# Optimization experiments

Hardware: AMD Instinct MI355X
Metric: run time of the kernel (lower is better)

## Reference

```python
import jax, jax.numpy as jnp
import numpy as np

C = 1.0      # base manifold curvature (Lorentz c)
C_E = 1.0    # expert manifold curvature (all experts init to c=1.0)
K = 1        # n_activated_experts (top-k)
SCALE = 2.0  # LResNet scale for shared-expert combine
EPS = 1e-8


def _lorentz_swiglu(x, W1, W3, W2, c_mid, c_out, prescale):
    """LorentzExpert / LorentzFeedForward: SwiGLU on space coords with Lorentz time lift.
    x: [T, D] (full Lorentz vector). W1,W3: [I-1, D]; W2: [D-1, I]. Returns [T, D]."""
    if prescale:
        x = x * np.float32(np.sqrt(C_E / C))  # x * sqrt(c_expert / c)
    s1 = jax.nn.silu(x @ W1.T)                 # [T, I-1] w1(x, return_space=True)
    s3 = x @ W3.T                              # [T, I-1] w3(x, return_space=True)
    sp = s1 * s3                               # gated space part
    t = jnp.sqrt(jnp.clip((sp * sp).sum(-1, keepdims=True) + c_mid, EPS))
    h = jnp.concatenate([t, sp], axis=-1)      # [T, I] point on expert manifold
    o = h @ W2.T                               # [T, D-1] w2 space output
    ot = jnp.sqrt(jnp.clip((o * o).sum(-1, keepdims=True) + c_out, EPS))
    return jnp.concatenate([ot, o], axis=-1)   # [T, D] on base manifold


def setup_inputs() -> dict:
    key = jax.random.key(0)
    ks = jax.random.split(key, 9)
    T, D, E, I = 2048, 1024, 8, 1024
    x = jax.random.normal(ks[0], (T, D), jnp.float32)
    gate_w = jax.random.normal(ks[1], (E, D - 1), jnp.float32) / np.sqrt(D - 1)
    gate_b = jax.random.normal(ks[2], (E,), jnp.float32) * 0.01
    W1 = jax.random.normal(ks[3], (E, I - 1, D), jnp.float32) / np.sqrt(D)
    W3 = jax.random.normal(ks[4], (E, I - 1, D), jnp.float32) / np.sqrt(D)
    W2 = jax.random.normal(ks[5], (E, D - 1, I), jnp.float32) / np.sqrt(I)
    Ws1 = jax.random.normal(ks[6], (I - 1, D), jnp.float32) / np.sqrt(D)
    Ws3 = jax.random.normal(ks[7], (I - 1, D), jnp.float32) / np.sqrt(D)
    Ws2 = jax.random.normal(ks[8], (D - 1, I), jnp.float32) / np.sqrt(I)
    return {"x": x, "gate_w": gate_w, "gate_b": gate_b, "W1": W1, "W3": W3,
            "W2": W2, "Ws1": Ws1, "Ws3": Ws3, "Ws2": Ws2}


def reference(x, gate_w, gate_b, W1, W3, W2, Ws1, Ws3, Ws2):
    T, D = x.shape
    E = gate_w.shape[0]
    # ---- Gate (softmax scoring, n_groups == 1, route_scale == 1.0) ----
    logits = x[:, 1:] @ gate_w.T                                    # [T, E]
    scores = jax.nn.softmax(logits.astype(jnp.float32), axis=-1)
    biased = scores + gate_b                                        # bias only affects routing
    _, idx = jax.lax.top_k(biased, K)                               # [T, K]
    weights = jnp.take_along_axis(scores, idx, axis=-1).astype(x.dtype)  # [T, K]
    # dense per-token expert gate weights [T, E]
    oh = jax.nn.one_hot(idx, E, dtype=x.dtype)                      # [T, K, E]
    gw = (oh * weights[..., None]).sum(axis=1)                      # [T, E]
    # ---- y init: project(zeros) -> [sqrt(c), 0, ..., 0] ----
    y0 = jnp.concatenate([jnp.full((T, 1), np.sqrt(C), x.dtype),
                          jnp.zeros((T, D - 1), x.dtype)], axis=-1)
    # ---- routed experts (dense reference: every expert on every token, masked combine) ----
    e_out = jax.vmap(lambda w1, w3, w2: _lorentz_swiglu(x, w1, w3, w2, C_E, C, True))(W1, W3, W2)  # [E, T, D]
    y = y0 + jnp.einsum('te,etd->td', gw, e_out)
    # ---- shared expert (LorentzFeedForward, stays on base manifold) ----
    z = _lorentz_swiglu(x, Ws1, Ws3, Ws2, C, C, False)
    # ---- LResNet weighted sum: normalize (z + scale*y) back to manifold ----
    comb = z + SCALE * y
    li = (comb[:, 1:] ** 2).sum(-1, keepdims=True) - comb[:, :1] ** 2  # Lorentz inner <comb,comb>
    out = np.float32(np.sqrt(C)) * comb / jnp.sqrt(jnp.clip(jnp.abs(li), EPS))
    return out
```

## Files before the change

kernel.cpp:

```cpp
#include <hip/hip_runtime.h>

typedef __bf16 bf16;
typedef __attribute__((ext_vector_type(8))) __bf16 bf16x8;
typedef __attribute__((ext_vector_type(4))) float floatx4;

#define TOK 2048
#define DD  1024
#define NE  8
#define LDA 40
#define MAXSLOT 72

__device__ __forceinline__ uint4 pack_bf8(float4 a, float4 b) {
  union { bf16 h[8]; uint4 u; } p;
  p.h[0] = (bf16)a.x; p.h[1] = (bf16)a.y; p.h[2] = (bf16)a.z; p.h[3] = (bf16)a.w;
  p.h[4] = (bf16)b.x; p.h[5] = (bf16)b.y; p.h[6] = (bf16)b.z; p.h[7] = (bf16)b.w;
  return p.u;
}

__global__ __launch_bounds__(256) void gate_cvt_kernel(
    const float* __restrict__ x, const float* __restrict__ gate_w,
    const float* __restrict__ gate_b, bf16* __restrict__ x_bf,
    int* __restrict__ eidx, float* __restrict__ ewgt)
{
  const int t = blockIdx.x, tid = threadIdx.x;
  const float4 v = ((const float4*)(x + (size_t)t * DD))[tid];
  union { bf16 h[4]; uint2 u; } pk;
  pk.h[0] = (bf16)v.x; pk.h[1] = (bf16)v.y; pk.h[2] = (bf16)v.z; pk.h[3] = (bf16)v.w;
  ((uint2*)(x_bf + (size_t)t * DD))[tid] = pk.u;

  float acc[NE];
#pragma unroll
  for (int e = 0; e < NE; ++e) acc[e] = 0.f;
  const float vv[4] = {v.x, v.y, v.z, v.w};
#pragma unroll
  for (int i = 0; i < 4; ++i) {
    const int d = tid * 4 + i;
    if (d >= 1) {
#pragma unroll
      for (int e = 0; e < NE; ++e) acc[e] += vv[i] * gate_w[e * (DD - 1) + d - 1];
    }
  }
#pragma unroll
  for (int off = 32; off > 0; off >>= 1) {
#pragma unroll
    for (int e = 0; e < NE; ++e) acc[e] += __shfl_down(acc[e], off);
  }
  __shared__ float red[4][NE];
  const int wid = tid >> 6, lane = tid & 63;
  if (lane == 0) {
#pragma unroll
    for (int e = 0; e < NE; ++e) red[wid][e] = acc[e];
  }
  __syncthreads();
  if (tid == 0) {
    float lg[NE];
#pragma unroll
    for (int e = 0; e < NE; ++e) lg[e] = red[0][e] + red[1][e] + red[2][e] + red[3][e];
    float m = lg[0];
    for (int e = 1; e < NE; ++e) m = fmaxf(m, lg[e]);
    float ex[NE], s = 0.f;
    for (int e = 0; e < NE; ++e) { ex[e] = expf(lg[e] - m); s += ex[e]; }
    const float inv = 1.f / s;
    int best = 0; float bb = ex[0] * inv + gate_b[0];
    for (int e = 1; e < NE; ++e) {
      const float b = ex[e] * inv + gate_b[e];
      if (b > bb) { bb = b; best = e; }
    }
    eidx[t] = best;
    ewgt[t] = ex[best] * inv;
  }
}

__global__ __launch_bounds__(256) void route_kernel(
    const int* __restrict__ eidx, int* __restrict__ perm,
    int* __restrict__ pos_of, int4* __restrict__ wl, int* __restrict__ wl_n)
{
  __shared__ int cnt[NE], off[NE], bas[NE + 1];
  const int tid = threadIdx.x;
  if (tid < NE) cnt[tid] = 0;
  __syncthreads();
  for (int t = tid; t < TOK; t += 256) atomicAdd(&cnt[eidx[t]], 1);
  __syncthreads();
  if (tid == 0) {
    int run = 0;
    for (int e = 0; e < NE; ++e) { bas[e] = run; off[e] = run; run += cnt[e]; }
    bas[NE] = run;
    int n = 0;
    for (int e = 0; e < NE; ++e)
      for (int r0 = 0; r0 < cnt[e]; r0 += 64) {
        int rows = cnt[e] - r0; if (rows > 64) rows = 64;
        wl[n++] = make_int4(bas[e] + r0, rows, e, 0);
      }
    for (int r0 = 0; r0 < TOK; r0 += 64) wl[n++] = make_int4(r0, 64, NE, 0);
    *wl_n = n;
  }
  __syncthreads();
  for (int t = tid; t < TOK; t += 256) {
    const int e = eidx[t];
    const int p = atomicAdd(&off[e], 1);
    perm[p] = t;
    pos_of[t] = p;
  }
}

__global__ __launch_bounds__(256) void mlp1_kernel(
    const bf16* __restrict__ x_bf,
    const float* __restrict__ W1, const float* __restrict__ W3,
    const float* __restrict__ Ws1, const float* __restrict__ Ws3,
    const int* __restrict__ perm, const int4* __restrict__ wl,
    const int* __restrict__ wl_n,
    bf16* __restrict__ h_r, bf16* __restrict__ h_s,
    float* __restrict__ ss_r, float* __restrict__ ss_z)
{
  const int bid = blockIdx.x;
  const int slot = bid >> 4, nt = bid & 15;
  if (slot >= *wl_n) return;
  const int4 wle = wl[slot];
  const int mbase = wle.x, rows = wle.y, eid = wle.z;
  const int tid = threadIdx.x;
  const bool routed = (eid < NE);
  const float* w1p = routed ? W1 + (size_t)eid * 1023 * 1024 : Ws1;
  const float* w3p = routed ? W3 + (size_t)eid * 1023 * 1024 : Ws3;
  bf16* hbuf  = routed ? h_r : h_s;
  float* ssbuf = routed ? ss_r : ss_z;
  const int n0 = nt * 64;

  __shared__ __align__(16) bf16 As[64 * LDA];
  __shared__ __align__(16) bf16 B1s[64 * LDA];
  __shared__ __align__(16) bf16 B3s[64 * LDA];
  __shared__ int toks[64];

  if (tid < 64) {
    int r = tid < rows ? tid : rows - 1;
    toks[tid] = routed ? perm[mbase + r] : (mbase + r);
  }
  __syncthreads();

  const int arow = tid >> 2, acol = (tid & 3) * 8;
  const bf16* aptr = x_bf + (size_t)toks[arow] * DD + acol;
  bf16* const alds = As + arow * LDA + acol;

  const int brow = tid >> 2, bcol = (tid & 3) * 8;
  int bn = n0 + brow; if (bn > 1022) bn = 1022;
  const float* b1ptr = w1p + (size_t)bn * 1024 + bcol;
  const float* b3ptr = w3p + (size_t)bn * 1024 + bcol;
  bf16* const b1lds = B1s + brow * LDA + bcol;
  bf16* const b3lds = B3s + brow * LDA + bcol;

  const int wid = tid >> 6, lane = tid & 63;
  const int wc = wid * 16;
  const int lrow = lane & 15, quad = lane >> 4;

  const floatx4 fz = {0.f, 0.f, 0.f, 0.f};
  floatx4 acc1[4], acc3[4];
#pragma unroll
  for (int mi = 0; mi < 4; ++mi) { acc1[mi] = fz; acc3[mi] = fz; }

  uint4  a0  = *(const uint4*)(aptr);
  float4 f10 = *(const float4*)(b1ptr);
  float4 f11 = *(const float4*)(b1ptr + 4);
  float4 f30 = *(const float4*)(b3ptr);
  float4 f31 = *(const float4*)(b3ptr + 4);

  for (int k0 = 0; k0 < 1024; k0 += 32) {
    __syncthreads();
    *(uint4*)alds  = a0;
    *(uint4*)b1lds = pack_bf8(f10, f11);
    *(uint4*)b3lds = pack_bf8(f30, f31);
    __syncthreads();
    const int kn = (k0 + 32 < 1024) ? (k0 + 32) : 0;
    a0  = *(const uint4*)(aptr + kn);
    f10 = *(const float4*)(b1ptr + kn);
    f11 = *(const float4*)(b1ptr + kn + 4);
    f30 = *(const float4*)(b3ptr + kn);
    f31 = *(const float4*)(b3ptr + kn + 4);

    bf16x8 af[4], b1f, b3f;
#pragma unroll
    for (int mi = 0; mi < 4; ++mi)
      af[mi] = *(const bf16x8*)(As + (mi * 16 + lrow) * LDA + quad * 8);
    b1f = *(const bf16x8*)(B1s + (wc + lrow) * LDA + quad * 8);
    b3f = *(const bf16x8*)(B3s + (wc + lrow) * LDA + quad * 8);
#pragma unroll
    for (int mi = 0; mi < 4; ++mi) {
      acc1[mi] = __builtin_amdgcn_mfma_f32_16x16x32_bf16(af[mi], b1f, acc1[mi], 0, 0, 0);
      acc3[mi] = __builtin_amdgcn_mfma_f32_16x16x32_bf16(af[mi], b3f, acc3[mi], 0, 0, 0);
    }
  }

  const int n = n0 + wc + lrow;
#pragma unroll
  for (int mi = 0; mi < 4; ++mi) {
#pragma unroll
    for (int r = 0; r < 4; ++r) {
      const int row = mi * 16 + quad * 4 + r;
      const bool ok = (row < rows) && (n < 1023);
      const float s1 = acc1[mi][r];
      const float s3 = acc3[mi][r];
      const float sp = (s1 / (1.f + __expf(-s1))) * s3;
      float ssum = ok ? sp * sp : 0.f;
      if (ok) hbuf[(size_t)(mbase + row) * 1024 + 1 + n] = (bf16)sp;
      ssum += __shfl_xor(ssum, 1);
      ssum += __shfl_xor(ssum, 2);
      ssum += __shfl_xor(ssum, 4);
      ssum += __shfl_xor(ssum, 8);
      if (lrow == 0 && row < rows) atomicAdd(ssbuf + mbase + row, ssum);
    }
  }
}

__global__ __launch_bounds__(256) void finalize_t_kernel(
    const float* __restrict__ ss_r, const float* __restrict__ ss_z,
    bf16* __restrict__ h_r, bf16* __restrict__ h_s)
{
  const int i = blockIdx.x * 256 + threadIdx.x;
  if (i < TOK) {
    h_r[(size_t)i * 1024] = (bf16)sqrtf(ss_r[i] + 1.0f);
    h_s[(size_t)i * 1024] = (bf16)sqrtf(ss_z[i] + 1.0f);
  }
}

__global__ __launch_bounds__(256) void mlp2_kernel(
    const bf16* __restrict__ h_r, const bf16* __restrict__ h_s,
    const float* __restrict__ W2, const float* __restrict__ Ws2,
    const int4* __restrict__ wl, const int* __restrict__ wl_n,
    float* __restrict__ o_r, float* __restrict__ o_s,
    float* __restrict__ ss_or, float* __restrict__ ss_oz)
{
  const int bid = blockIdx.x;
  const int slot = bid >> 4, nt = bid & 15;
  if (slot >= *wl_n) return;
  const int4 wle = wl[slot];
  const int mbase = wle.x, rows = wle.y, eid = wle.z;
  const int tid = threadIdx.x;
  const bool routed = (eid < NE);
  const float* wp = routed ? W2 + (size_t)eid * 1023 * 1024 : Ws2;
  const bf16* abuf = routed ? h_r : h_s;
  float* obuf  = routed ? o_r : o_s;
  float* ssbuf = routed ? ss_or : ss_oz;
  const int n0 = nt * 64;

  __shared__ __align__(16) bf16 As[64 * LDA];
  __shared__ __align__(16) bf16 Bs[64 * LDA];

  const int arow = tid >> 2, acol = (tid & 3) * 8;
  const int ar = arow < rows ? arow : rows - 1;
  const bf16* aptr = abuf + (size_t)(mbase + ar) * 1024 + acol;
  bf16* const alds = As + arow * LDA + acol;

  const int brow = tid >> 2, bcol = (tid & 3) * 8;
  int bn = n0 + brow; if (bn > 1022) bn = 1022;
  const float* bptr = wp + (size_t)bn * 1024 + bcol;
  bf16* const blds = Bs + brow * LDA + bcol;

  const int wid = tid >> 6, lane = tid & 63;
  const int wc = wid * 16;
  const int lrow = lane & 15, quad = lane >> 4;

  const floatx4 fz = {0.f, 0.f, 0.f, 0.f};
  floatx4 acc[4];
#pragma unroll
  for (int mi = 0; mi < 4; ++mi) acc[mi] = fz;

  uint4  a0 = *(const uint4*)(aptr);
  float4 f0 = *(const float4*)(bptr);
  float4 f1 = *(const float4*)(bptr + 4);

  for (int k0 = 0; k0 < 1024; k0 += 32) {
    __syncthreads();
    *(uint4*)alds = a0;
    *(uint4*)blds = pack_bf8(f0, f1);
    __syncthreads();
    const int kn = (k0 + 32 < 1024) ? (k0 + 32) : 0;
    a0 = *(const uint4*)(aptr + kn);
    f0 = *(const float4*)(bptr + kn);
    f1 = *(const float4*)(bptr + kn + 4);

    bf16x8 af[4], bfr;
#pragma unroll
    for (int mi = 0; mi < 4; ++mi)
      af[mi] = *(const bf16x8*)(As + (mi * 16 + lrow) * LDA + quad * 8);
    bfr = *(const bf16x8*)(Bs + (wc + lrow) * LDA + quad * 8);
#pragma unroll
    for (int mi = 0; mi < 4; ++mi)
      acc[mi] = __builtin_amdgcn_mfma_f32_16x16x32_bf16(af[mi], bfr, acc[mi], 0, 0, 0);
  }

  const int n = n0 + wc + lrow;
#pragma unroll
  for (int mi = 0; mi < 4; ++mi) {
#pragma unroll
    for (int r = 0; r < 4; ++r) {
      const int row = mi * 16 + quad * 4 + r;
      const bool ok = (row < rows) && (n < 1023);
      const float v = acc[mi][r];
      float ssum = ok ? v * v : 0.f;
      if (ok) obuf[(size_t)(mbase + row) * 1024 + n] = v;
      ssum += __shfl_xor(ssum, 1);
      ssum += __shfl_xor(ssum, 2);
      ssum += __shfl_xor(ssum, 4);
      ssum += __shfl_xor(ssum, 8);
      if (lrow == 0 && row < rows) atomicAdd(ssbuf + mbase + row, ssum);
    }
  }
}

__global__ __launch_bounds__(256) void combine_kernel(
    const float* __restrict__ o_r, const float* __restrict__ o_s,
    const float* __restrict__ ss_or, const float* __restrict__ ss_oz,
    const int* __restrict__ pos_of, const float* __restrict__ wgt,
    float* __restrict__ out)
{
  const int t = blockIdx.x, tid = threadIdx.x;
  const int p = pos_of[t];
  const float w = wgt[t];
  const float4 oz = ((const float4*)(o_s + (size_t)t * 1024))[tid];
  const float4 oe = ((const float4*)(o_r + (size_t)p * 1024))[tid];
  const float tw = 2.f * w;
  float c0 = oz.x + tw * oe.x;
  float c1 = oz.y + tw * oe.y;
  float c2 = oz.z + tw * oe.z;
  float c3 = (tid == 255) ? 0.f : (oz.w + tw * oe.w);
  float ssum = c0 * c0 + c1 * c1 + c2 * c2 + c3 * c3;
#pragma unroll
  for (int off = 32; off > 0; off >>= 1) ssum += __shfl_down(ssum, off);
  __shared__ float rs[4];
  if ((tid & 63) == 0) rs[tid >> 6] = ssum;
  __syncthreads();
  const float space2 = rs[0] + rs[1] + rs[2] + rs[3];
  const float comb0 = sqrtf(ss_oz[t] + 1.f) + 2.f + 2.f * w * sqrtf(ss_or[p] + 1.f);
  const float li = space2 - comb0 * comb0;
  const float inv = 1.f / sqrtf(fmaxf(fabsf(li), 1e-8f));
  float* orow = out + (size_t)t * 1024;
  const int j = 1 + tid * 4;
  orow[j]     = c0 * inv;
  orow[j + 1] = c1 * inv;
  orow[j + 2] = c2 * inv;
  if (tid != 255) orow[j + 3] = c3 * inv;
  if (tid == 0) orow[0] = comb0 * inv;
}

extern "C" void kernel_launch(void* const* d_in, const int* in_sizes, int n_in,
                              void* d_out, int out_size, void* d_ws, size_t ws_size,
                              hipStream_t stream) {
  const float* x      = (const float*)d_in[0];
  const float* gate_w = (const float*)d_in[1];
  const float* gate_b = (const float*)d_in[2];
  const float* W1     = (const float*)d_in[3];
  const float* W3     = (const float*)d_in[4];
  const float* W2     = (const float*)d_in[5];
  const float* Ws1    = (const float*)d_in[6];
  const float* Ws3    = (const float*)d_in[7];
  const float* Ws2    = (const float*)d_in[8];
  float* out = (float*)d_out;

  char* ws = (char*)d_ws;
  size_t off = 0;
  auto alloc = [&](size_t bytes) {
    void* p = ws + off;
    off += (bytes + 255) & ~(size_t)255;
    return p;
  };
  bf16*  x_bf = (bf16*) alloc((size_t)TOK * 1024 * 2);
  bf16*  h_r  = (bf16*) alloc((size_t)TOK * 1024 * 2);
  bf16*  h_s  = (bf16*) alloc((size_t)TOK * 1024 * 2);
  float* o_r  = (float*)alloc((size_t)TOK * 1024 * 4);
  float* o_s  = (float*)alloc((size_t)TOK * 1024 * 4);
  float* ss   = (float*)alloc((size_t)4 * TOK * 4);
  int*   eidx = (int*)  alloc((size_t)TOK * 4);
  float* ewgt = (float*)alloc((size_t)TOK * 4);
  int*   perm = (int*)  alloc((size_t)TOK * 4);
  int*   posf = (int*)  alloc((size_t)TOK * 4);
  int4*  wl   = (int4*) alloc((size_t)MAXSLOT * 16);
  int*   wln  = (int*)  alloc(16);

  float* ss_r  = ss;
  float* ss_z  = ss + TOK;
  float* ss_or = ss + 2 * TOK;
  float* ss_oz = ss + 3 * TOK;

  hipMemsetAsync(ss, 0, (size_t)4 * TOK * 4, stream);
  gate_cvt_kernel<<<TOK, 256, 0, stream>>>(x, gate_w, gate_b, x_bf, eidx, ewgt);
  route_kernel<<<1, 256, 0, stream>>>(eidx, perm, posf, wl, wln);
  mlp1_kernel<<<MAXSLOT * 16, 256, 0, stream>>>(x_bf, W1, W3, Ws1, Ws3, perm, wl, wln,
                                                h_r, h_s, ss_r, ss_z);
  finalize_t_kernel<<<8, 256, 0, stream>>>(ss_r, ss_z, h_r, h_s);
  mlp2_kernel<<<MAXSLOT * 16, 256, 0, stream>>>(h_r, h_s, W2, Ws2, wl, wln,
                                                o_r, o_s, ss_or, ss_oz);
  combine_kernel<<<TOK, 256, 0, stream>>>(o_r, o_s, ss_or, ss_oz, posf, ewgt, out);
}
```

Before: 285.1 us.

## Pre-convert weights to bf16 and use larger LDS-direct tiled GEMMs

Adds a kernel that converts all expert and shared weights to bf16 once per call, with W1/W3 rows interleaved so a single GEMM produces both gate and up projections. mlp1 now uses 128x128 tiles and mlp2 uses 64x128 tiles, with global_load_lds into XOR-swizzled LDS and 4x4 or 2x4 MFMA blocks per wave. This cuts the repeated fp32 weight reads and in-loop conversion, and raises MFMA work per byte of LDS traffic. The memset is folded into the gate kernel. The cost is a full weight-conversion pass and extra workspace, with no double buffering of loads.

```diff
diff --git a/kernel.cpp b/kernel.cpp
--- a/kernel.cpp
+++ b/kernel.cpp
@@ -7,8 +7,16 @@
 #define TOK 2048
 #define DD  1024
 #define NE  8
-#define LDA 40
-#define MAXSLOT 72
+#define S1MAX 48
+#define S2MAX 80
+
+#define MFMA16(A,B,C) __builtin_amdgcn_mfma_f32_16x16x32_bf16(A,B,C,0,0,0)
+
+__device__ __forceinline__ void load_lds16(const bf16* g, bf16* l) {
+  __builtin_amdgcn_global_load_lds(
+      (const __attribute__((address_space(1))) void*)g,
+      (__attribute__((address_space(3))) void*)l, 16, 0, 0);
+}
 
 __device__ __forceinline__ uint4 pack_bf8(float4 a, float4 b) {
   union { bf16 h[8]; uint4 u; } p;
@@ -17,12 +25,45 @@
   return p.u;
 }
 
+#define NCVT (8*2046 + 2046 + 8*1023 + 1023)
+__global__ __launch_bounds__(128) void convert_kernel(
+    const float* __restrict__ W1, const float* __restrict__ W3,
+    const float* __restrict__ W2, const float* __restrict__ Ws1,
+    const float* __restrict__ Ws3, const float* __restrict__ Ws2,
+    bf16* __restrict__ w13, bf16* __restrict__ ws13,
+    bf16* __restrict__ w2b, bf16* __restrict__ ws2b)
+{
+  const int r = blockIdx.x, tid = threadIdx.x;
+  const float* src; bf16* dst;
+  if (r < 8 * 2046) {
+    const int e = r / 2046, q = r % 2046;
+    src = ((q & 1) ? W3 : W1) + ((size_t)e * 1023 + (q >> 1)) * 1024;
+    dst = w13 + (size_t)r * 1024;
+  } else if (r < 8 * 2046 + 2046) {
+    const int q = r - 8 * 2046;
+    src = ((q & 1) ? Ws3 : Ws1) + (size_t)(q >> 1) * 1024;
+    dst = ws13 + (size_t)q * 1024;
+  } else if (r < 8 * 2046 + 2046 + 8 * 1023) {
+    const int q = r - (8 * 2046 + 2046);
+    src = W2 + (size_t)q * 1024;
+    dst = w2b + (size_t)q * 1024;
+  } else {
+    const int q = r - (8 * 2046 + 2046 + 8 * 1023);
+    src = Ws2 + (size_t)q * 1024;
+    dst = ws2b + (size_t)q * 1024;
+  }
+  const float4 f0 = ((const float4*)src)[tid * 2];
+  const float4 f1 = ((const float4*)src)[tid * 2 + 1];
+  ((uint4*)dst)[tid] = pack_bf8(f0, f1);
+}
+
 __global__ __launch_bounds__(256) void gate_cvt_kernel(
     const float* __restrict__ x, const float* __restrict__ gate_w,
     const float* __restrict__ gate_b, bf16* __restrict__ x_bf,
-    int* __restrict__ eidx, float* __restrict__ ewgt)
+    int* __restrict__ eidx, float* __restrict__ ewgt, float* __restrict__ ss)
 {
   const int t = blockIdx.x, tid = threadIdx.x;
+  if (tid < 4) ss[tid * TOK + t] = 0.f;
   const float4 v = ((const float4*)(x + (size_t)t * DD))[tid];
   union { bf16 h[4]; uint2 u; } pk;
   pk.h[0] = (bf16)v.x; pk.h[1] = (bf16)v.y; pk.h[2] = (bf16)v.z; pk.h[3] = (bf16)v.w;
@@ -73,7 +114,8 @@
 
 __global__ __launch_bounds__(256) void route_kernel(
     const int* __restrict__ eidx, int* __restrict__ perm,
-    int* __restrict__ pos_of, int4* __restrict__ wl, int* __restrict__ wl_n)
+    int* __restrict__ pos_of, int4* __restrict__ wl1, int* __restrict__ n1,
+    int4* __restrict__ wl2, int* __restrict__ n2)
 {
   __shared__ int cnt[NE], off[NE], bas[NE + 1];
   const int tid = threadIdx.x;
@@ -87,12 +129,20 @@
     bas[NE] = run;
     int n = 0;
     for (int e = 0; e < NE; ++e)
+      for (int r0 = 0; r0 < cnt[e]; r0 += 128) {
+        int rows = cnt[e] - r0; if (rows > 128) rows = 128;
+        wl1[n++] = make_int4(bas[e] + r0, rows, e, 0);
+      }
+    for (int r0 = 0; r0 < TOK; r0 += 128) wl1[n++] = make_int4(r0, 128, NE, 0);
+    *n1 = n;
+    n = 0;
+    for (int e = 0; e < NE; ++e)
       for (int r0 = 0; r0 < cnt[e]; r0 += 64) {
         int rows = cnt[e] - r0; if (rows > 64) rows = 64;
-        wl[n++] = make_int4(bas[e] + r0, rows, e, 0);
+        wl2[n++] = make_int4(bas[e] + r0, rows, e, 0);
       }
-    for (int r0 = 0; r0 < TOK; r0 += 64) wl[n++] = make_int4(r0, 64, NE, 0);
-    *wl_n = n;
+    for (int r0 = 0; r0 < TOK; r0 += 64) wl2[n++] = make_int4(r0, 64, NE, 0);
+    *n2 = n;
   }
   __syncthreads();
   for (int t = tid; t < TOK; t += 256) {
@@ -104,9 +154,8 @@
 }
 
 __global__ __launch_bounds__(256) void mlp1_kernel(
-    const bf16* __restrict__ x_bf,
-    const float* __restrict__ W1, const float* __restrict__ W3,
-    const float* __restrict__ Ws1, const float* __restrict__ Ws3,
+    const bf16* __restrict__ x_bf, const bf16* __restrict__ w13,
+    const bf16* __restrict__ ws13,
     const int* __restrict__ perm, const int4* __restrict__ wl,
     const int* __restrict__ wl_n,
     bf16* __restrict__ h_r, bf16* __restrict__ h_s,
@@ -119,92 +168,107 @@
   const int mbase = wle.x, rows = wle.y, eid = wle.z;
   const int tid = threadIdx.x;
   const bool routed = (eid < NE);
-  const float* w1p = routed ? W1 + (size_t)eid * 1023 * 1024 : Ws1;
-  const float* w3p = routed ? W3 + (size_t)eid * 1023 * 1024 : Ws3;
+  const bf16* bmat = routed ? w13 + (size_t)eid * 2046 * 1024 : ws13;
   bf16* hbuf  = routed ? h_r : h_s;
   float* ssbuf = routed ? ss_r : ss_z;
-  const int n0 = nt * 64;
-
-  __shared__ __align__(16) bf16 As[64 * LDA];
-  __shared__ __align__(16) bf16 B1s[64 * LDA];
-  __shared__ __align__(16) bf16 B3s[64 * LDA];
-  __shared__ int toks[64];
-
-  if (tid < 64) {
+
+  __shared__ __align__(16) bf16 As[128 * 64];
+  __shared__ __align__(16) bf16 Bs[128 * 64];
+  __shared__ int toks[128];
+  if (tid < 128) {
     int r = tid < rows ? tid : rows - 1;
     toks[tid] = routed ? perm[mbase + r] : (mbase + r);
   }
   __syncthreads();
 
-  const int arow = tid >> 2, acol = (tid & 3) * 8;
-  const bf16* aptr = x_bf + (size_t)toks[arow] * DD + acol;
-  bf16* const alds = As + arow * LDA + acol;
-
-  const int brow = tid >> 2, bcol = (tid & 3) * 8;
-  int bn = n0 + brow; if (bn > 1022) bn = 1022;
-  const float* b1ptr = w1p + (size_t)bn * 1024 + bcol;
-  const float* b3ptr = w3p + (size_t)bn * 1024 + bcol;
-  bf16* const b1lds = B1s + brow * LDA + bcol;
-  bf16* const b3lds = B3s + brow * LDA + bcol;
-
   const int wid = tid >> 6, lane = tid & 63;
-  const int wc = wid * 16;
-  const int lrow = lane & 15, quad = lane >> 4;
+  const int srow = lane >> 3;
+  const int kbg  = (lane & 7) ^ (srow & 7);
+  const bf16 *aG0, *aG1, *aG2, *aG3, *bG0, *bG1, *bG2, *bG3;
+  bf16 *aL0, *aL1, *aL2, *aL3, *bL0, *bL1, *bL2, *bL3;
+  {
+    const int r0 = wid * 32;
+    aG0 = x_bf + (size_t)toks[r0 +  0 + srow] * 1024 + kbg * 8;
+    aG1 = x_bf + (size_t)toks[r0 +  8 + srow] * 1024 + kbg * 8;
+    aG2 = x_bf + (size_t)toks[r0 + 16 + srow] * 1024 + kbg * 8;
+    aG3 = x_bf + (size_t)toks[r0 + 24 + srow] * 1024 + kbg * 8;
+    aL0 = As + (r0 +  0) * 64; aL1 = As + (r0 +  8) * 64;
+    aL2 = As + (r0 + 16) * 64; aL3 = As + (r0 + 24) * 64;
+    int b0 = nt * 128 + r0 + 0 + srow;  if (b0 > 2045) b0 = 2045;
+    int b1 = nt * 128 + r0 + 8 + srow;  if (b1 > 2045) b1 = 2045;
+    int b2 = nt * 128 + r0 + 16 + srow; if (b2 > 2045) b2 = 2045;
+    int b3 = nt * 128 + r0 + 24 + srow; if (b3 > 2045) b3 = 2045;
+    bG0 = bmat + (size_t)b0 * 1024 + kbg * 8;
+    bG1 = bmat + (size_t)b1 * 1024 + kbg * 8;
+    bG2 = bmat + (size_t)b2 * 1024 + kbg * 8;
+    bG3 = bmat + (size_t)b3 * 1024 + kbg * 8;
+    bL0 = Bs + (r0 +  0) * 64; bL1 = Bs + (r0 +  8) * 64;
+    bL2 = Bs + (r0 + 16) * 64; bL3 = Bs + (r0 + 24) * 64;
+  }
+
+  const int lrow = lane & 15, quad = lane >> 4, sw = lane & 7;
+  const int wrow = (wid >> 1) * 64, wcol = (wid & 1) * 64;
+  int aoff[4], boff[4], koff[2];
+#pragma unroll
+  for (int mi = 0; mi < 4; ++mi) aoff[mi] = (wrow + mi * 16 + lrow) * 64;
+#pragma unroll
+  for (int ni = 0; ni < 4; ++ni) boff[ni] = (wcol + ni * 16 + lrow) * 64;
+#pragma unroll
+  for (int kk = 0; kk < 2; ++kk) koff[kk] = ((kk * 4 + quad) ^ sw) * 8;
 
   const floatx4 fz = {0.f, 0.f, 0.f, 0.f};
-  floatx4 acc1[4], acc3[4];
-#pragma unroll
-  for (int mi = 0; mi < 4; ++mi) { acc1[mi] = fz; acc3[mi] = fz; }
-
-  uint4  a0  = *(const uint4*)(aptr);
-  float4 f10 = *(const float4*)(b1ptr);
-  float4 f11 = *(const float4*)(b1ptr + 4);
-  float4 f30 = *(const float4*)(b3ptr);
-  float4 f31 = *(const float4*)(b3ptr + 4);
-
-  for (int k0 = 0; k0 < 1024; k0 += 32) {
+  floatx4 acc[4][4];
+#pragma unroll
+  for (int mi = 0; mi < 4; ++mi)
+#pragma unroll
+    for (int ni = 0; ni < 4; ++ni) acc[mi][ni] = fz;
+
+  for (int ke = 0; ke < 1024; ke += 64) {
+    load_lds16(aG0 + ke, aL0); load_lds16(aG1 + ke, aL1);
+    load_lds16(aG2 + ke, aL2); load_lds16(aG3 + ke, aL3);
+    load_lds16(bG0 + ke, bL0); load_lds16(bG1 + ke, bL1);
+    load_lds16(bG2 + ke, bL2); load_lds16(bG3 + ke, bL3);
     __syncthreads();
-    *(uint4*)alds  = a0;
-    *(uint4*)b1lds = pack_bf8(f10, f11);
-    *(uint4*)b3lds = pack_bf8(f30, f31);
+#pragma unroll
+    for (int kk = 0; kk < 2; ++kk) {
+      bf16x8 av[4], bv[4];
+#pragma unroll
+      for (int mi = 0; mi < 4; ++mi) av[mi] = *(const bf16x8*)(As + aoff[mi] + koff[kk]);
+#pragma unroll
+      for (int ni = 0; ni < 4; ++ni) bv[ni] = *(const bf16x8*)(Bs + boff[ni] + koff[kk]);
+#pragma unroll
+      for (int mi = 0; mi < 4; ++mi)
+#pragma unroll
+        for (int ni = 0; ni < 4; ++ni)
+          acc[mi][ni] = MFMA16(av[mi], bv[ni], acc[mi][ni]);
+    }
     __syncthreads();
-    const int kn = (k0 + 32 < 1024) ? (k0 + 32) : 0;
-    a0  = *(const uint4*)(aptr + kn);
-    f10 = *(const float4*)(b1ptr + kn);
-    f11 = *(const float4*)(b1ptr + kn + 4);
-    f30 = *(const float4*)(b3ptr + kn);
-    f31 = *(const float4*)(b3ptr + kn + 4);
-
-    bf16x8 af[4], b1f, b3f;
-#pragma unroll
-    for (int mi = 0; mi < 4; ++mi)
-      af[mi] = *(const bf16x8*)(As + (mi * 16 + lrow) * LDA + quad * 8);
-    b1f = *(const bf16x8*)(B1s + (wc + lrow) * LDA + quad * 8);
-    b3f = *(const bf16x8*)(B3s + (wc + lrow) * LDA + quad * 8);
-#pragma unroll
-    for (int mi = 0; mi < 4; ++mi) {
-      acc1[mi] = __builtin_amdgcn_mfma_f32_16x16x32_bf16(af[mi], b1f, acc1[mi], 0, 0, 0);
-      acc3[mi] = __builtin_amdgcn_mfma_f32_16x16x32_bf16(af[mi], b3f, acc3[mi], 0, 0, 0);
-    }
-  }
-
-  const int n = n0 + wc + lrow;
+  }
+
 #pragma unroll
   for (int mi = 0; mi < 4; ++mi) {
 #pragma unroll
     for (int r = 0; r < 4; ++r) {
-      const int row = mi * 16 + quad * 4 + r;
-      const bool ok = (row < rows) && (n < 1023);
-      const float s1 = acc1[mi][r];
-      const float s3 = acc3[mi][r];
-      const float sp = (s1 / (1.f + __expf(-s1))) * s3;
-      float ssum = ok ? sp * sp : 0.f;
-      if (ok) hbuf[(size_t)(mbase + row) * 1024 + 1 + n] = (bf16)sp;
+      const int row = wrow + mi * 16 + quad * 4 + r;
+      const bool rowok = row < rows;
+      float ssum = 0.f;
+#pragma unroll
+      for (int ni = 0; ni < 4; ++ni) {
+        const float c = acc[mi][ni][r];
+        const float partner = __shfl_xor(c, 1);
+        const float s1 = (lane & 1) ? partner : c;
+        const float s3 = (lane & 1) ? c : partner;
+        const float sp = (s1 / (1.f + __expf(-s1))) * s3;
+        const int P = (nt * 128 + wcol + ni * 16 + lrow) >> 1;
+        const bool ok = rowok && ((lane & 1) == 0) && (P < 1023);
+        if (ok) hbuf[(size_t)(mbase + row) * 1024 + 1 + P] = (bf16)sp;
+        ssum += ok ? sp * sp : 0.f;
+      }
       ssum += __shfl_xor(ssum, 1);
       ssum += __shfl_xor(ssum, 2);
       ssum += __shfl_xor(ssum, 4);
       ssum += __shfl_xor(ssum, 8);
-      if (lrow == 0 && row < rows) atomicAdd(ssbuf + mbase + row, ssum);
+      if (lrow == 0 && rowok) atomicAdd(ssbuf + mbase + row, ssum);
     }
   }
 }
@@ -222,85 +286,110 @@
 
 __global__ __launch_bounds__(256) void mlp2_kernel(
     const bf16* __restrict__ h_r, const bf16* __restrict__ h_s,
-    const float* __restrict__ W2, const float* __restrict__ Ws2,
+    const bf16* __restrict__ w2b, const bf16* __restrict__ ws2b,
     const int4* __restrict__ wl, const int* __restrict__ wl_n,
     float* __restrict__ o_r, float* __restrict__ o_s,
     float* __restrict__ ss_or, float* __restrict__ ss_oz)
 {
   const int bid = blockIdx.x;
-  const int slot = bid >> 4, nt = bid & 15;
+  const int slot = bid >> 3, nt = bid & 7;
   if (slot >= *wl_n) return;
   const int4 wle = wl[slot];
   const int mbase = wle.x, rows = wle.y, eid = wle.z;
   const int tid = threadIdx.x;
   const bool routed = (eid < NE);
-  const float* wp = routed ? W2 + (size_t)eid * 1023 * 1024 : Ws2;
   const bf16* abuf = routed ? h_r : h_s;
+  const bf16* bmat = routed ? w2b + (size_t)eid * 1023 * 1024 : ws2b;
   float* obuf  = routed ? o_r : o_s;
   float* ssbuf = routed ? ss_or : ss_oz;
-  const int n0 = nt * 64;
-
-  __shared__ __align__(16) bf16 As[64 * LDA];
-  __shared__ __align__(16) bf16 Bs[64 * LDA];
-
-  const int arow = tid >> 2, acol = (tid & 3) * 8;
-  const int ar = arow < rows ? arow : rows - 1;
-  const bf16* aptr = abuf + (size_t)(mbase + ar) * 1024 + acol;
-  bf16* const alds = As + arow * LDA + acol;
-
-  const int brow = tid >> 2, bcol = (tid & 3) * 8;
-  int bn = n0 + brow; if (bn > 1022) bn = 1022;
-  const float* bptr = wp + (size_t)bn * 1024 + bcol;
-  bf16* const blds = Bs + brow * LDA + bcol;
+  const int n0 = nt * 128;
+
+  __shared__ __align__(16) bf16 As[64 * 64];
+  __shared__ __align__(16) bf16 Bs[128 * 64];
 
   const int wid = tid >> 6, lane = tid & 63;
-  const int wc = wid * 16;
-  const int lrow = lane & 15, quad = lane >> 4;
+  const int srow = lane >> 3;
+  const int kbg  = (lane & 7) ^ (srow & 7);
+  const bf16 *aG0, *aG1, *bG0, *bG1, *bG2, *bG3;
+  bf16 *aL0, *aL1, *bL0, *bL1, *bL2, *bL3;
+  {
+    int ra0 = wid * 16 + 0 + srow; if (ra0 >= rows) ra0 = rows - 1;
+    int ra1 = wid * 16 + 8 + srow; if (ra1 >= rows) ra1 = rows - 1;
+    aG0 = abuf + (size_t)(mbase + ra0) * 1024 + kbg * 8;
+    aG1 = abuf + (size_t)(mbase + ra1) * 1024 + kbg * 8;
+    aL0 = As + (wid * 16 + 0) * 64;
+    aL1 = As + (wid * 16 + 8) * 64;
+    const int r0 = wid * 32;
+    int b0 = n0 + r0 + 0 + srow;  if (b0 > 1022) b0 = 1022;
+    int b1 = n0 + r0 + 8 + srow;  if (b1 > 1022) b1 = 1022;
+    int b2 = n0 + r0 + 16 + srow; if (b2 > 1022) b2 = 1022;
+    int b3 = n0 + r0 + 24 + srow; if (b3 > 1022) b3 = 1022;
+    bG0 = bmat + (size_t)b0 * 1024 + kbg * 8;
+    bG1 = bmat + (size_t)b1 * 1024 + kbg * 8;
+    bG2 = bmat + (size_t)b2 * 1024 + kbg * 8;
+    bG3 = bmat + (size_t)b3 * 1024 + kbg * 8;
+    bL0 = Bs + (r0 +  0) * 64; bL1 = Bs + (r0 +  8) * 64;
+    bL2 = Bs + (r0 + 16) * 64; bL3 = Bs + (r0 + 24) * 64;
+  }
+
+  const int lrow = lane & 15, quad = lane >> 4, sw = lane & 7;
+  const int wrow = (wid >> 1) * 32, wcol = (wid & 1) * 64;
+  int aoff[2], boff[4], koff[2];
+#pragma unroll
+  for (int mi = 0; mi < 2; ++mi) aoff[mi] = (wrow + mi * 16 + lrow) * 64;
+#pragma unroll
+  for (int ni = 0; ni < 4; ++ni) boff[ni] = (wcol + ni * 16 + lrow) * 64;
+#pragma unroll
+  for (int kk = 0; kk < 2; ++kk) koff[kk] = ((kk * 4 + quad) ^ sw) * 8;
 
   const floatx4 fz = {0.f, 0.f, 0.f, 0.f};
-  floatx4 acc[4];
-#pragma unroll
-  for (int mi = 0; mi < 4; ++mi) acc[mi] = fz;
-
-  uint4  a0 = *(const uint4*)(aptr);
-  float4 f0 = *(const float4*)(bptr);
-  float4 f1 = *(const float4*)(bptr + 4);
-
-  for (int k0 = 0; k0 < 1024; k0 += 32) {
+  floatx4 acc[2][4];
+#pragma unroll
+  for (int mi = 0; mi < 2; ++mi)
+#pragma unroll
+    for (int ni = 0; ni < 4; ++ni) acc[mi][ni] = fz;
+
+  for (int ke = 0; ke < 1024; ke += 64) {
+    load_lds16(aG0 + ke, aL0); load_lds16(aG1 + ke, aL1);
+    load_lds16(bG0 + ke, bL0); load_lds16(bG1 + ke, bL1);
+    load_lds16(bG2 + ke, bL2); load_lds16(bG3 + ke, bL3);
     __syncthreads();
-    *(uint4*)alds = a0;
-    *(uint4*)blds = pack_bf8(f0, f1);
+#pragma unroll
+    for (int kk = 0; kk < 2; ++kk) {
+      bf16x8 av[2], bv[4];
+#pragma unroll
+      for (int mi = 0; mi < 2; ++mi) av[mi] = *(const bf16x8*)(As + aoff[mi] + koff[kk]);
+#pragma unroll
+      for (int ni = 0; ni < 4; ++ni) bv[ni] = *(const bf16x8*)(Bs + boff[ni] + koff[kk]);
+#pragma unroll
+      for (int mi = 0; mi < 2; ++mi)
+#pragma unroll
+        for (int ni = 0; ni < 4; ++ni)
+          acc[mi][ni] = MFMA16(av[mi], bv[ni], acc[mi][ni]);
+    }
     __syncthreads();
-    const int kn = (k0 + 32 < 1024) ? (k0 + 32) : 0;
-    a0 = *(const uint4*)(aptr + kn);
-    f0 = *(const float4*)(bptr + kn);
-    f1 = *(const float4*)(bptr + kn + 4);
-
-    bf16x8 af[4], bfr;
-#pragma unroll
-    for (int mi = 0; mi < 4; ++mi)
-      af[mi] = *(const bf16x8*)(As + (mi * 16 + lrow) * LDA + quad * 8);
-    bfr = *(const bf16x8*)(Bs + (wc + lrow) * LDA + quad * 8);
-#pragma unroll
-    for (int mi = 0; mi < 4; ++mi)
-      acc[mi] = __builtin_amdgcn_mfma_f32_16x16x32_bf16(af[mi], bfr, acc[mi], 0, 0, 0);
-  }
-
-  const int n = n0 + wc + lrow;
-#pragma unroll
-  for (int mi = 0; mi < 4; ++mi) {
+  }
+
+#pragma unroll
+  for (int mi = 0; mi < 2; ++mi) {
 #pragma unroll
     for (int r = 0; r < 4; ++r) {
-      const int row = mi * 16 + quad * 4 + r;
-      const bool ok = (row < rows) && (n < 1023);
-      const float v = acc[mi][r];
-      float ssum = ok ? v * v : 0.f;
-      if (ok) obuf[(size_t)(mbase + row) * 1024 + n] = v;
+      const int row = wrow + mi * 16 + quad * 4 + r;
+      const bool rowok = row < rows;
+      float ssum = 0.f;
+#pragma unroll
+      for (int ni = 0; ni < 4; ++ni) {
+        const float v = acc[mi][ni][r];
+        const int n = n0 + wcol + ni * 16 + lrow;
+        const bool ok = rowok && (n < 1023);
+        if (ok) obuf[(size_t)(mbase + row) * 1024 + n] = v;
+        ssum += ok ? v * v : 0.f;
+      }
       ssum += __shfl_xor(ssum, 1);
       ssum += __shfl_xor(ssum, 2);
       ssum += __shfl_xor(ssum, 4);
       ssum += __shfl_xor(ssum, 8);
-      if (lrow == 0 && row < rows) atomicAdd(ssbuf + mbase + row, ssum);
+      if (lrow == 0 && rowok) atomicAdd(ssbuf + mbase + row, ssum);
     }
   }
 }
@@ -371,21 +460,27 @@
   float* ewgt = (float*)alloc((size_t)TOK * 4);
   int*   perm = (int*)  alloc((size_t)TOK * 4);
   int*   posf = (int*)  alloc((size_t)TOK * 4);
-  int4*  wl   = (int4*) alloc((size_t)MAXSLOT * 16);
-  int*   wln  = (int*)  alloc(16);
+  int4*  wl1  = (int4*) alloc((size_t)S1MAX * 16);
+  int4*  wl2  = (int4*) alloc((size_t)S2MAX * 16);
+  int*   wn   = (int*)  alloc(32);
+  bf16*  w13  = (bf16*) alloc((size_t)8 * 2046 * 1024 * 2);
+  bf16*  ws13 = (bf16*) alloc((size_t)2046 * 1024 * 2);
+  bf16*  w2b  = (bf16*) alloc((size_t)8 * 1023 * 1024 * 2);
+  bf16*  ws2b = (bf16*) alloc((size_t)1023 * 1024 * 2);
 
   float* ss_r  = ss;
   float* ss_z  = ss + TOK;
   float* ss_or = ss + 2 * TOK;
   float* ss_oz = ss + 3 * TOK;
 
-  hipMemsetAsync(ss, 0, (size_t)4 * TOK * 4, stream);
-  gate_cvt_kernel<<<TOK, 256, 0, stream>>>(x, gate_w, gate_b, x_bf, eidx, ewgt);
-  route_kernel<<<1, 256, 0, stream>>>(eidx, perm, posf, wl, wln);
-  mlp1_kernel<<<MAXSLOT * 16, 256, 0, stream>>>(x_bf, W1, W3, Ws1, Ws3, perm, wl, wln,
-                                                h_r, h_s, ss_r, ss_z);
+  convert_kernel<<<NCVT, 128, 0, stream>>>(W1, W3, W2, Ws1, Ws3, Ws2,
+                                           w13, ws13, w2b, ws2b);
+  gate_cvt_kernel<<<TOK, 256, 0, stream>>>(x, gate_w, gate_b, x_bf, eidx, ewgt, ss);
+  route_kernel<<<1, 256, 0, stream>>>(eidx, perm, posf, wl1, wn, wl2, wn + 1);
+  mlp1_kernel<<<S1MAX * 16, 256, 0, stream>>>(x_bf, w13, ws13, perm, wl1, wn,
+                                              h_r, h_s, ss_r, ss_z);
   finalize_t_kernel<<<8, 256, 0, stream>>>(ss_r, ss_z, h_r, h_s);
-  mlp2_kernel<<<MAXSLOT * 16, 256, 0, stream>>>(h_r, h_s, W2, Ws2, wl, wln,
-                                                o_r, o_s, ss_or, ss_oz);
+  mlp2_kernel<<<S2MAX * 8, 256, 0, stream>>>(h_r, h_s, w2b, ws2b, wl2, wn + 1,
+                                             o_r, o_s, ss_or, ss_oz);
   combine_kernel<<<TOK, 256, 0, stream>>>(o_r, o_s, ss_or, ss_oz, posf, ewgt, out);
 }
```

Measured after the change: 252.6 us. 1.13x faster.
